# Kernel optimization log

Hardware: AMD Instinct MI355X
Metric: run time of the kernel (lower is better)

The kernel has to match this reference:

```python
import jax, jax.numpy as jnp
import numpy as np

B, T, D, H, C = 256, 512, 128, 512, 10

def setup_inputs() -> dict:
    key = jax.random.key(0)
    ks = jax.random.split(key, 16)
    def kn(k, shape):  # kaiming-normal-ish init (gain irrelevant for correctness)
        fan_in = shape[-1]
        return jax.random.normal(k, shape, dtype=jnp.float32) * (1.0 / np.sqrt(fan_in))
    return {
        "x": jax.random.randint(ks[0], (B, T), 0, 3),
        "emb": jax.random.normal(ks[1], (3, D), dtype=jnp.float32),
        "Wfx": kn(ks[2], (H, D)), "Wfh": kn(ks[3], (H, H)), "bf": jnp.zeros((H,), jnp.float32),
        "Wix": kn(ks[4], (H, D)), "Wih": kn(ks[5], (H, H)), "bi": jnp.zeros((H,), jnp.float32),
        "Wox": kn(ks[6], (H, D)), "Woh": kn(ks[7], (H, H)), "bo": jnp.zeros((H,), jnp.float32),
        "Wcx": kn(ks[8], (H, D)), "bc": jnp.zeros((H,), jnp.float32),
        "Wph": kn(ks[9], (C, H)), "bp": jnp.zeros((C,), jnp.float32),
    }

def _forward(x, emb, Wfx, Wfh, bf, Wix, Wih, bi, Wox, Woh, bo, Wcx, bc, Wph, bp):
    xe = emb[x]  # [B, T, D]
    # Precompute input-to-gate projections as one big batched matmul each.
    fx = jnp.einsum('btd,hd->bth', xe, Wfx) + bf  # [B, T, H]
    ix = jnp.einsum('btd,hd->bth', xe, Wix) + bi
    ox = jnp.einsum('btd,hd->bth', xe, Wox) + bo
    cx = jnp.einsum('btd,hd->bth', xe, Wcx) + bc
    gates = jnp.stack([fx, ix, ox, cx], axis=0).transpose(2, 1, 0, 3)  # [T, B, 4, H]

    def step(carry, g):
        c, _ = carry
        gf, gi, go, gc = g[:, 0], g[:, 1], g[:, 2], g[:, 3]  # each [B, H]
        f = jax.nn.sigmoid(gf + c @ Wfh.T)
        i = jax.nn.sigmoid(gi + c @ Wih.T)
        o = jax.nn.sigmoid(go + c @ Woh.T)
        c_new = jax.nn.sigmoid(gc) * i + c * f
        h = jnp.tanh(c_new) * o
        return (c_new, h), None

    c0 = jnp.zeros((x.shape[0], Wfh.shape[0]), jnp.float32)
    (c_fin, h_fin), _ = jax.lax.scan(step, (c0, c0), gates)
    p = h_fin @ Wph.T + bp
    return jax.nn.log_softmax(p, axis=1)

def reference(x, emb, Wfx, Wfh, bf, Wix, Wih, bi, Wox, Woh, bo, Wcx, bc, Wph, bp):
    return _forward(x, emb, Wfx, Wfh, bf, Wix, Wih, bi, Wox, Woh, bo, Wcx, bc, Wph, bp)
```

## Files before the change

kernel.cpp:

```cpp
#include <hip/hip_runtime.h>
#include <stdint.h>

#define TLEN 512
#define HDIM 512
#define DDIM 128
#define NCLS 10

typedef float f32x4 __attribute__((ext_vector_type(4)));
typedef short bf16x8 __attribute__((ext_vector_type(8)));
typedef unsigned long long u64;

__device__ __forceinline__ unsigned short f2bf(float f) {
  union { float f; unsigned u; } v; v.f = f;
  return (unsigned short)((v.u + 0x7FFFu + ((v.u >> 16) & 1u)) >> 16);
}
__device__ __forceinline__ float bf2f(unsigned short h) {
  union { unsigned u; float f; } v; v.u = ((unsigned)h) << 16; return v.f;
}
__device__ __forceinline__ float sigm(float x) {
  return __builtin_amdgcn_rcpf(1.0f + __expf(-x));
}
__device__ __forceinline__ u64 ald(const u64* p) {
  return __hip_atomic_load(p, __ATOMIC_RELAXED, __HIP_MEMORY_SCOPE_AGENT);
}
__device__ __forceinline__ void ast16(unsigned short* p, unsigned short v) {
  __hip_atomic_store(p, v, __ATOMIC_RELAXED, __HIP_MEMORY_SCOPE_AGENT);
}
__device__ __forceinline__ void astd(unsigned* p, unsigned v) {
  __hip_atomic_store(p, v, __ATOMIC_RELAXED, __HIP_MEMORY_SCOPE_AGENT);
}

__global__ void k_gates(const float* __restrict__ emb,
                        const float* __restrict__ Wfx, const float* __restrict__ bf_,
                        const float* __restrict__ Wix, const float* __restrict__ bi_,
                        const float* __restrict__ Wcx, const float* __restrict__ bc_,
                        const float* __restrict__ Wox, const float* __restrict__ bo_,
                        float* __restrict__ G) {
  int tid = blockIdx.x * 256 + threadIdx.x;
  int h = tid & (HDIM - 1);
  int v = (tid >> 9) % 3;
  int g = tid / (3 * HDIM);
  const float* W; const float* bb;
  if (g == 0)      { W = Wfx; bb = bf_; }
  else if (g == 1) { W = Wix; bb = bi_; }
  else if (g == 2) { W = Wcx; bb = bc_; }
  else             { W = Wox; bb = bo_; }
  const float* e = emb + v * DDIM;
  const float* w = W + h * DDIM;
  float s = bb[h];
  #pragma unroll 8
  for (int d = 0; d < DDIM; ++d) s += e[d] * w[d];
  if (g == 2) s = sigm(s);
  G[tid] = s;
}

__global__ void k_pack_fi(const float* __restrict__ Wfh, const float* __restrict__ Wih,
                          unsigned short* __restrict__ pk) {
  int tid = blockIdx.x * 256 + threadIdx.x;
  int l  = tid & 63;
  int kt = (tid >> 6) & 15;
  int g  = (tid >> 10) & 1;
  int nt = (tid >> 11) & 3;
  int hs = (tid >> 13) & 7;
  int n  = hs * 64 + nt * 16 + (l & 15);
  int k0 = kt * 32 + (l >> 4) * 8;
  const float* src = (g ? Wih : Wfh) + n * HDIM + k0;
  unsigned short* dst = pk + (size_t)tid * 8;
  #pragma unroll
  for (int e = 0; e < 8; ++e) dst[e] = f2bf(src[e]);
}

__global__ void k_pack_o(const float* __restrict__ Woh, unsigned short* __restrict__ pk) {
  int tid = blockIdx.x * 256 + threadIdx.x;
  int l  = tid & 63;
  int kt = (tid >> 6) & 15;
  int nt = (tid >> 10) & 3;
  int hs = (tid >> 12) & 7;
  int n  = hs * 64 + nt * 16 + (l & 15);
  int k0 = kt * 32 + (l >> 4) * 8;
  const float* src = Woh + n * HDIM + k0;
  unsigned short* dst = pk + (size_t)tid * 8;
  #pragma unroll
  for (int e = 0; e < 8; ++e) dst[e] = f2bf(src[e]);
}

__global__ __launch_bounds__(256, 1)
void k_scan(const int* __restrict__ x, const float* __restrict__ G,
            const unsigned short* __restrict__ pk2,
            const unsigned short* __restrict__ pko,
            char* __restrict__ cbuf, unsigned* __restrict__ flg,
            unsigned short* __restrict__ hfin) {
  __shared__ float gts[12][68];
  __shared__ unsigned char xv[16][516];
  __shared__ uint4 lds_a[16][64];

  const int tid  = threadIdx.x;
  const int lane = tid & 63;
  const int w    = tid >> 6;
  const int bt   = blockIdx.x & 15;
  const int hs   = blockIdx.x >> 4;

  for (int j = tid; j < 12 * 64; j += 256) {
    int gv = j >> 6, c = j & 63;
    gts[gv][c] = G[gv * HDIM + hs * 64 + c];
  }
  for (int j = tid; j < 16 * TLEN; j += 256) {
    int r = j >> 9, tt = j & (TLEN - 1);
    xv[r][tt] = (unsigned char)x[(bt * 16 + r) * TLEN + tt];
  }

  bf16x8 wf[16], wi[16];
  {
    const bf16x8* ws = (const bf16x8*)pk2 + (size_t)((hs * 4 + w) * 2) * (16 * 64) + lane;
    #pragma unroll
    for (int kt = 0; kt < 16; ++kt) { wf[kt] = ws[kt * 64]; wi[kt] = ws[(16 + kt) * 64]; }
  }

  bf16x8 afr[16];
  #pragma unroll
  for (int kt = 0; kt < 16; ++kt) afr[kt] = bf16x8{0,0,0,0,0,0,0,0};

  float cf[4] = {0.f, 0.f, 0.f, 0.f};
  const int rgrp = (lane >> 4) * 4;
  const int coll = lane & 15;
  const int col  = w * 16 + coll;
  const int colb = (hs * 64 + col) * 2;
  const int rowb = (lane & 15) * 1024 + (lane >> 4) * 16;
  const f32x4 zz = {0.f, 0.f, 0.f, 0.f};

  __syncthreads();

  for (int t = 0; t < TLEN - 1; ++t) {
    f32x4 af = zz, ai = zz;
    #pragma unroll
    for (int kt = 0; kt < 16; ++kt) {
      af = __builtin_amdgcn_mfma_f32_16x16x32_bf16(afr[kt], wf[kt], af, 0, 0, 0);
      ai = __builtin_amdgcn_mfma_f32_16x16x32_bf16(afr[kt], wi[kt], ai, 0, 0, 0);
    }
    const unsigned tg = (unsigned)(t + 1);
    const int par = (int)(tg & 1);
    char* dbase = cbuf + par * 262144 + bt * 16384;

    #pragma unroll
    for (int r = 0; r < 4; ++r) {
      int vv = xv[rgrp + r][t];
      float fg = sigm(af[r] + gts[0 + vv][col]);
      float ig = sigm(ai[r] + gts[3 + vv][col]);
      float sc = gts[6 + vv][col];
      float cn = sc * ig + cf[r] * fg;
      cf[r] = cn;
      ast16((unsigned short*)(dbase + (rgrp + r) * 1024 + colb), f2bf(cn));
    }
    __syncthreads();

    unsigned* fl = flg + (par * 16 + bt) * 16;
    if (tid == 0) astd(fl + hs, tg);

    const u64 pat2 = ((u64)tg << 32) | (u64)tg;
    const u64* fp = (const u64*)fl;
    u64 g0, g1, g2, g3;
    do {
      g0 = ald(fp + 0); g1 = ald(fp + 1); g2 = ald(fp + 2); g3 = ald(fp + 3);
    } while (((g0 ^ pat2) | (g1 ^ pat2) | (g2 ^ pat2) | (g3 ^ pat2)) != 0ULL);
    asm volatile("" ::: "memory");

    const char* rb = dbase + rowb;
    #pragma unroll
    for (int i = 0; i < 4; ++i) {
      const int kt = (w << 2) | i;
      const u64* p = (const u64*)(rb + kt * 64);
      u64 lo = ald(p + 0), hi = ald(p + 1);
      uint4 q;
      q.x = (unsigned)lo; q.y = (unsigned)(lo >> 32);
      q.z = (unsigned)hi; q.w = (unsigned)(hi >> 32);
      lds_a[kt][lane] = q;
    }
    __syncthreads();
    #pragma unroll
    for (int kt = 0; kt < 16; ++kt) {
      union { uint4 q; bf16x8 v; } u;
      u.q = lds_a[kt][lane];
      afr[kt] = u.v;
    }
  }

  {
    const int t = TLEN - 1;
    bf16x8 wo[16];
    const bf16x8* os = (const bf16x8*)pko + (size_t)(hs * 4 + w) * (16 * 64) + lane;
    #pragma unroll
    for (int kt = 0; kt < 16; ++kt) wo[kt] = os[kt * 64];
    f32x4 af = zz, ai = zz, ao = zz;
    #pragma unroll
    for (int kt = 0; kt < 16; ++kt) {
      af = __builtin_amdgcn_mfma_f32_16x16x32_bf16(afr[kt], wf[kt], af, 0, 0, 0);
      ai = __builtin_amdgcn_mfma_f32_16x16x32_bf16(afr[kt], wi[kt], ai, 0, 0, 0);
      ao = __builtin_amdgcn_mfma_f32_16x16x32_bf16(afr[kt], wo[kt], ao, 0, 0, 0);
    }
    #pragma unroll
    for (int r = 0; r < 4; ++r) {
      int vv = xv[rgrp + r][t];
      float fg = sigm(af[r] + gts[0 + vv][col]);
      float ig = sigm(ai[r] + gts[3 + vv][col]);
      float sc = gts[6 + vv][col];
      float cn = sc * ig + cf[r] * fg;
      float og = sigm(ao[r] + gts[9 + vv][col]);
      float hv = tanhf(cn) * og;
      hfin[(bt * 16 + rgrp + r) * HDIM + hs * 64 + col] = f2bf(hv);
    }
  }
}

__global__ __launch_bounds__(64)
void k_head(const unsigned short* __restrict__ hfin, const float* __restrict__ Wph,
            const float* __restrict__ bp, float* __restrict__ out) {
  const int b = blockIdx.x;
  const int lane = threadIdx.x;
  float acc[NCLS];
  #pragma unroll
  for (int c = 0; c < NCLS; ++c) acc[c] = 0.f;
  const unsigned short* hrow = hfin + (size_t)b * HDIM;
  for (int k = lane; k < HDIM; k += 64) {
    float hv = bf2f(hrow[k]);
    #pragma unroll
    for (int c = 0; c < NCLS; ++c) acc[c] += hv * Wph[c * HDIM + k];
  }
  #pragma unroll
  for (int c = 0; c < NCLS; ++c)
    #pragma unroll
    for (int off = 32; off > 0; off >>= 1)
      acc[c] += __shfl_down(acc[c], off, 64);
  if (lane == 0) {
    float p[NCLS]; float m = -1e30f;
    #pragma unroll
    for (int c = 0; c < NCLS; ++c) { p[c] = acc[c] + bp[c]; m = fmaxf(m, p[c]); }
    float s = 0.f;
    #pragma unroll
    for (int c = 0; c < NCLS; ++c) s += __expf(p[c] - m);
    const float ls = __logf(s);
    #pragma unroll
    for (int c = 0; c < NCLS; ++c) out[b * NCLS + c] = p[c] - m - ls;
  }
}

extern "C" void kernel_launch(void* const* d_in, const int* in_sizes, int n_in,
                              void* d_out, int out_size, void* d_ws, size_t ws_size,
                              hipStream_t stream) {
  const int*   x   = (const int*)d_in[0];
  const float* emb = (const float*)d_in[1];
  const float* Wfx = (const float*)d_in[2];
  const float* Wfh = (const float*)d_in[3];
  const float* bf_ = (const float*)d_in[4];
  const float* Wix = (const float*)d_in[5];
  const float* Wih = (const float*)d_in[6];
  const float* bi_ = (const float*)d_in[7];
  const float* Wox = (const float*)d_in[8];
  const float* Woh = (const float*)d_in[9];
  const float* bo_ = (const float*)d_in[10];
  const float* Wcx = (const float*)d_in[11];
  const float* bc_ = (const float*)d_in[12];
  const float* Wph = (const float*)d_in[13];
  const float* bp_ = (const float*)d_in[14];

  char* ws = (char*)d_ws;
  float*          G    = (float*)(ws);
  unsigned short* hfin = (unsigned short*)(ws + 32768);
  char*           cbuf = (char*)(ws + 524288);
  unsigned*       flg  = (unsigned*)(ws + 1048576);
  unsigned short* pk2  = (unsigned short*)(ws + 1114112);
  unsigned short* pko  = (unsigned short*)(ws + 2162688);

  hipMemsetAsync(flg, 0, 2048, stream);
  hipLaunchKernelGGL(k_gates,   dim3(24),  dim3(256), 0, stream,
                     emb, Wfx, bf_, Wix, bi_, Wcx, bc_, Wox, bo_, G);
  hipLaunchKernelGGL(k_pack_fi, dim3(256), dim3(256), 0, stream, Wfh, Wih, pk2);
  hipLaunchKernelGGL(k_pack_o,  dim3(128), dim3(256), 0, stream, Woh, pko);
  hipLaunchKernelGGL(k_scan,    dim3(128), dim3(256), 0, stream, x, G, pk2, pko, cbuf, flg, hfin);
  hipLaunchKernelGGL(k_head,    dim3(256), dim3(64),  0, stream, hfin, Wph, bp_, (float*)d_out);
}
```

Baseline: 1.469 ms.

## Replace flag barrier with step-tagged data words polled directly

Each cell-state value is now stored as a 32-bit word that holds the bf16 value with the step index in its upper half. Consumers poll the data itself with sc1 global loads until every tag matches, then pack the halves into bf16 fragments with perm. This removes the per-step __syncthreads, the flag store and the separate flag poll, cutting one round-trip of cross-block latency per timestep. The cost is twice the exchange traffic and spin-polling on the whole data tile. The final step's Woh load is also moved after the f/i MFMAs.

```diff
diff --git a/kernel.cpp b/kernel.cpp
--- a/kernel.cpp
+++ b/kernel.cpp
@@ -20,15 +20,14 @@
 __device__ __forceinline__ float sigm(float x) {
   return __builtin_amdgcn_rcpf(1.0f + __expf(-x));
 }
-__device__ __forceinline__ u64 ald(const u64* p) {
-  return __hip_atomic_load(p, __ATOMIC_RELAXED, __HIP_MEMORY_SCOPE_AGENT);
-}
-__device__ __forceinline__ void ast16(unsigned short* p, unsigned short v) {
+__device__ __forceinline__ void astw(unsigned* p, unsigned v) {
   __hip_atomic_store(p, v, __ATOMIC_RELAXED, __HIP_MEMORY_SCOPE_AGENT);
 }
-__device__ __forceinline__ void astd(unsigned* p, unsigned v) {
-  __hip_atomic_store(p, v, __ATOMIC_RELAXED, __HIP_MEMORY_SCOPE_AGENT);
-}
+
+#define GLOAD_SC1(dst, addr) \
+  asm volatile("global_load_dwordx4 %0, %1, off sc1" : "=&v"(dst) : "v"(addr))
+#define VMWAIT() do { asm volatile("s_waitcnt vmcnt(0)" ::: "memory"); \
+                      __builtin_amdgcn_sched_barrier(0); } while (0)
 
 __global__ void k_gates(const float* __restrict__ emb,
                         const float* __restrict__ Wfx, const float* __restrict__ bf_,
@@ -88,7 +87,7 @@
 void k_scan(const int* __restrict__ x, const float* __restrict__ G,
             const unsigned short* __restrict__ pk2,
             const unsigned short* __restrict__ pko,
-            char* __restrict__ cbuf, unsigned* __restrict__ flg,
+            char* __restrict__ cbuf,
             unsigned short* __restrict__ hfin) {
   __shared__ float gts[12][68];
   __shared__ unsigned char xv[16][516];
@@ -100,12 +99,12 @@
   const int bt   = blockIdx.x & 15;
   const int hs   = blockIdx.x >> 4;
 
-  for (int j = tid; j < 12 * 64; j += 256) {
-    int gv = j >> 6, c = j & 63;
+  for (int jj = tid; jj < 12 * 64; jj += 256) {
+    int gv = jj >> 6, c = jj & 63;
     gts[gv][c] = G[gv * HDIM + hs * 64 + c];
   }
-  for (int j = tid; j < 16 * TLEN; j += 256) {
-    int r = j >> 9, tt = j & (TLEN - 1);
+  for (int jj = tid; jj < 16 * TLEN; jj += 256) {
+    int r = jj >> 9, tt = jj & (TLEN - 1);
     xv[r][tt] = (unsigned char)x[(bt * 16 + r) * TLEN + tt];
   }
 
@@ -124,8 +123,10 @@
   const int rgrp = (lane >> 4) * 4;
   const int coll = lane & 15;
   const int col  = w * 16 + coll;
-  const int colb = (hs * 64 + col) * 2;
-  const int rowb = (lane & 15) * 1024 + (lane >> 4) * 16;
+  const int ktp  = 2 * hs + (col >> 5);
+  const int wrdo = col & 31;
+  const int pofs = ktp * 2048 + rgrp * 128 + wrdo * 4;
+  const int cofs = (lane & 15) * 128 + (lane >> 4) * 32;
   const f32x4 zz = {0.f, 0.f, 0.f, 0.f};
 
   __syncthreads();
@@ -137,9 +138,9 @@
       af = __builtin_amdgcn_mfma_f32_16x16x32_bf16(afr[kt], wf[kt], af, 0, 0, 0);
       ai = __builtin_amdgcn_mfma_f32_16x16x32_bf16(afr[kt], wi[kt], ai, 0, 0, 0);
     }
-    const unsigned tg = (unsigned)(t + 1);
-    const int par = (int)(tg & 1);
-    char* dbase = cbuf + par * 262144 + bt * 16384;
+    const unsigned tg  = (unsigned)(t + 1);
+    const unsigned tgh = tg << 16;
+    char* tbase = cbuf + (size_t)((tg & 1) * 16 + bt) * 32768;
 
     #pragma unroll
     for (int r = 0; r < 4; ++r) {
@@ -149,31 +150,56 @@
       float sc = gts[6 + vv][col];
       float cn = sc * ig + cf[r] * fg;
       cf[r] = cn;
-      ast16((unsigned short*)(dbase + (rgrp + r) * 1024 + colb), f2bf(cn));
-    }
-    __syncthreads();
-
-    unsigned* fl = flg + (par * 16 + bt) * 16;
-    if (tid == 0) astd(fl + hs, tg);
-
-    const u64 pat2 = ((u64)tg << 32) | (u64)tg;
-    const u64* fp = (const u64*)fl;
-    u64 g0, g1, g2, g3;
+      astw((unsigned*)(tbase + pofs + r * 128), tgh | (unsigned)f2bf(cn));
+    }
+
+    const char* qb = tbase + cofs;
+    uint4 d0, d1, d2, d3, d4, d5, d6, d7;
+    unsigned bad;
     do {
-      g0 = ald(fp + 0); g1 = ald(fp + 1); g2 = ald(fp + 2); g3 = ald(fp + 3);
-    } while (((g0 ^ pat2) | (g1 ^ pat2) | (g2 ^ pat2) | (g3 ^ pat2)) != 0ULL);
-    asm volatile("" ::: "memory");
-
-    const char* rb = dbase + rowb;
-    #pragma unroll
-    for (int i = 0; i < 4; ++i) {
-      const int kt = (w << 2) | i;
-      const u64* p = (const u64*)(rb + kt * 64);
-      u64 lo = ald(p + 0), hi = ald(p + 1);
+      GLOAD_SC1(d0, qb + ((w << 2) | 0) * 2048);
+      GLOAD_SC1(d1, qb + ((w << 2) | 0) * 2048 + 16);
+      GLOAD_SC1(d2, qb + ((w << 2) | 1) * 2048);
+      GLOAD_SC1(d3, qb + ((w << 2) | 1) * 2048 + 16);
+      GLOAD_SC1(d4, qb + ((w << 2) | 2) * 2048);
+      GLOAD_SC1(d5, qb + ((w << 2) | 2) * 2048 + 16);
+      GLOAD_SC1(d6, qb + ((w << 2) | 3) * 2048);
+      GLOAD_SC1(d7, qb + ((w << 2) | 3) * 2048 + 16);
+      VMWAIT();
+      unsigned m = 0;
+      m |= (d0.x ^ tgh) | (d0.y ^ tgh) | (d0.z ^ tgh) | (d0.w ^ tgh);
+      m |= (d1.x ^ tgh) | (d1.y ^ tgh) | (d1.z ^ tgh) | (d1.w ^ tgh);
+      m |= (d2.x ^ tgh) | (d2.y ^ tgh) | (d2.z ^ tgh) | (d2.w ^ tgh);
+      m |= (d3.x ^ tgh) | (d3.y ^ tgh) | (d3.z ^ tgh) | (d3.w ^ tgh);
+      m |= (d4.x ^ tgh) | (d4.y ^ tgh) | (d4.z ^ tgh) | (d4.w ^ tgh);
+      m |= (d5.x ^ tgh) | (d5.y ^ tgh) | (d5.z ^ tgh) | (d5.w ^ tgh);
+      m |= (d6.x ^ tgh) | (d6.y ^ tgh) | (d6.z ^ tgh) | (d6.w ^ tgh);
+      m |= (d7.x ^ tgh) | (d7.y ^ tgh) | (d7.z ^ tgh) | (d7.w ^ tgh);
+      bad = m & 0xFFFF0000u;
+    } while (__any(bad != 0));
+
+    {
       uint4 q;
-      q.x = (unsigned)lo; q.y = (unsigned)(lo >> 32);
-      q.z = (unsigned)hi; q.w = (unsigned)(hi >> 32);
-      lds_a[kt][lane] = q;
+      q.x = __builtin_amdgcn_perm(d0.y, d0.x, 0x05040100);
+      q.y = __builtin_amdgcn_perm(d0.w, d0.z, 0x05040100);
+      q.z = __builtin_amdgcn_perm(d1.y, d1.x, 0x05040100);
+      q.w = __builtin_amdgcn_perm(d1.w, d1.z, 0x05040100);
+      lds_a[(w << 2) | 0][lane] = q;
+      q.x = __builtin_amdgcn_perm(d2.y, d2.x, 0x05040100);
+      q.y = __builtin_amdgcn_perm(d2.w, d2.z, 0x05040100);
+      q.z = __builtin_amdgcn_perm(d3.y, d3.x, 0x05040100);
+      q.w = __builtin_amdgcn_perm(d3.w, d3.z, 0x05040100);
+      lds_a[(w << 2) | 1][lane] = q;
+      q.x = __builtin_amdgcn_perm(d4.y, d4.x, 0x05040100);
+      q.y = __builtin_amdgcn_perm(d4.w, d4.z, 0x05040100);
+      q.z = __builtin_amdgcn_perm(d5.y, d5.x, 0x05040100);
+      q.w = __builtin_amdgcn_perm(d5.w, d5.z, 0x05040100);
+      lds_a[(w << 2) | 2][lane] = q;
+      q.x = __builtin_amdgcn_perm(d6.y, d6.x, 0x05040100);
+      q.y = __builtin_amdgcn_perm(d6.w, d6.z, 0x05040100);
+      q.z = __builtin_amdgcn_perm(d7.y, d7.x, 0x05040100);
+      q.w = __builtin_amdgcn_perm(d7.w, d7.z, 0x05040100);
+      lds_a[(w << 2) | 3][lane] = q;
     }
     __syncthreads();
     #pragma unroll
@@ -186,17 +212,19 @@
 
   {
     const int t = TLEN - 1;
-    bf16x8 wo[16];
-    const bf16x8* os = (const bf16x8*)pko + (size_t)(hs * 4 + w) * (16 * 64) + lane;
-    #pragma unroll
-    for (int kt = 0; kt < 16; ++kt) wo[kt] = os[kt * 64];
     f32x4 af = zz, ai = zz, ao = zz;
     #pragma unroll
     for (int kt = 0; kt < 16; ++kt) {
       af = __builtin_amdgcn_mfma_f32_16x16x32_bf16(afr[kt], wf[kt], af, 0, 0, 0);
       ai = __builtin_amdgcn_mfma_f32_16x16x32_bf16(afr[kt], wi[kt], ai, 0, 0, 0);
+    }
+    bf16x8 wo[16];
+    const bf16x8* os = (const bf16x8*)pko + (size_t)(hs * 4 + w) * (16 * 64) + lane;
+    #pragma unroll
+    for (int kt = 0; kt < 16; ++kt) wo[kt] = os[kt * 64];
+    #pragma unroll
+    for (int kt = 0; kt < 16; ++kt)
       ao = __builtin_amdgcn_mfma_f32_16x16x32_bf16(afr[kt], wo[kt], ao, 0, 0, 0);
-    }
     #pragma unroll
     for (int r = 0; r < 4; ++r) {
       int vv = xv[rgrp + r][t];
@@ -266,15 +294,14 @@
   float*          G    = (float*)(ws);
   unsigned short* hfin = (unsigned short*)(ws + 32768);
   char*           cbuf = (char*)(ws + 524288);
-  unsigned*       flg  = (unsigned*)(ws + 1048576);
-  unsigned short* pk2  = (unsigned short*)(ws + 1114112);
-  unsigned short* pko  = (unsigned short*)(ws + 2162688);
-
-  hipMemsetAsync(flg, 0, 2048, stream);
+  unsigned short* pk2  = (unsigned short*)(ws + 1572864);
+  unsigned short* pko  = (unsigned short*)(ws + 2621440);
+
   hipLaunchKernelGGL(k_gates,   dim3(24),  dim3(256), 0, stream,
                      emb, Wfx, bf_, Wix, bi_, Wcx, bc_, Wox, bo_, G);
   hipLaunchKernelGGL(k_pack_fi, dim3(256), dim3(256), 0, stream, Wfh, Wih, pk2);
   hipLaunchKernelGGL(k_pack_o,  dim3(128), dim3(256), 0, stream, Woh, pko);
-  hipLaunchKernelGGL(k_scan,    dim3(128), dim3(256), 0, stream, x, G, pk2, pko, cbuf, flg, hfin);
+  hipLaunchKernelGGL(k_scan,    dim3(128), dim3(256), 0, stream,
+                     x, G, pk2, pko, cbuf, hfin);
   hipLaunchKernelGGL(k_head,    dim3(256), dim3(64),  0, stream, hfin, Wph, bp_, (float*)d_out);
 }
```

Result: slower. 2.012 ms (+37.0%).

## Add XCD-local fast path for inter-block step synchronization and state exchange

Applied to the files above, without the earlier changes.

At startup each block records its XCC_ID and checks whether all 8 blocks sharing a batch tile run on the same XCD. If they do, the cell state and step flags are also written and polled with sc0 (L2-coherent, XCD-local) loads and stores. This is meant to avoid the higher-latency device-scope path on every one of the 511 timesteps. A bounded spin falls back to a mirrored sc1/agent-scope buffer, which adds an extra store per element and relies on hardware-specific cache-scope semantics. The Woh load is also moved after the f/i MFMAs in the final step.

```diff
diff --git a/kernel.cpp b/kernel.cpp
--- a/kernel.cpp
+++ b/kernel.cpp
@@ -20,15 +20,26 @@
 __device__ __forceinline__ float sigm(float x) {
   return __builtin_amdgcn_rcpf(1.0f + __expf(-x));
 }
-__device__ __forceinline__ u64 ald(const u64* p) {
-  return __hip_atomic_load(p, __ATOMIC_RELAXED, __HIP_MEMORY_SCOPE_AGENT);
-}
 __device__ __forceinline__ void ast16(unsigned short* p, unsigned short v) {
   __hip_atomic_store(p, v, __ATOMIC_RELAXED, __HIP_MEMORY_SCOPE_AGENT);
 }
 __device__ __forceinline__ void astd(unsigned* p, unsigned v) {
   __hip_atomic_store(p, v, __ATOMIC_RELAXED, __HIP_MEMORY_SCOPE_AGENT);
 }
+__device__ __forceinline__ unsigned aldd(const unsigned* p) {
+  return __hip_atomic_load(p, __ATOMIC_RELAXED, __HIP_MEMORY_SCOPE_AGENT);
+}
+
+#define GLOAD_SC1(dst, addr) \
+  asm volatile("global_load_dwordx4 %0, %1, off sc1" : "=&v"(dst) : "v"(addr))
+#define GLOAD_SC0(dst, addr) \
+  asm volatile("global_load_dwordx4 %0, %1, off sc0" : "=&v"(dst) : "v"(addr))
+#define GSTORE16_SC0(addr, val) \
+  asm volatile("global_store_short %0, %1, off sc0" :: "v"(addr), "v"(val) : "memory")
+#define GSTORED_SC0(addr, val) \
+  asm volatile("global_store_dword %0, %1, off sc0" :: "v"(addr), "v"(val) : "memory")
+#define VMWAIT() do { asm volatile("s_waitcnt vmcnt(0)" ::: "memory"); \
+                      __builtin_amdgcn_sched_barrier(0); } while (0)
 
 __global__ void k_gates(const float* __restrict__ emb,
                         const float* __restrict__ Wfx, const float* __restrict__ bf_,
@@ -88,11 +99,14 @@
 void k_scan(const int* __restrict__ x, const float* __restrict__ G,
             const unsigned short* __restrict__ pk2,
             const unsigned short* __restrict__ pko,
-            char* __restrict__ cbuf, unsigned* __restrict__ flg,
+            char* __restrict__ bufB, unsigned* __restrict__ flgB,
+            char* __restrict__ bufA, unsigned* __restrict__ flgA,
+            unsigned* __restrict__ xcdtab,
             unsigned short* __restrict__ hfin) {
   __shared__ float gts[12][68];
   __shared__ unsigned char xv[16][516];
   __shared__ uint4 lds_a[16][64];
+  __shared__ int fastsh, fastok;
 
   const int tid  = threadIdx.x;
   const int lane = tid & 63;
@@ -100,12 +114,25 @@
   const int bt   = blockIdx.x & 15;
   const int hs   = blockIdx.x >> 4;
 
-  for (int j = tid; j < 12 * 64; j += 256) {
-    int gv = j >> 6, c = j & 63;
+  if (tid == 0) {
+    unsigned myx;
+    asm volatile("s_getreg_b32 %0, hwreg(HW_REG_XCC_ID)" : "=s"(myx));
+    astd(xcdtab + (hs * 16 + bt), (myx & 0xFFu) | 0x100u);
+    unsigned id0 = 0; int f = 1;
+    for (int k = 0; k < 8; ++k) {
+      unsigned v;
+      do { v = aldd(xcdtab + (k * 16 + bt)); } while (!(v & 0x100u));
+      if (k == 0) id0 = v; else f &= (v == id0);
+    }
+    fastsh = f; fastok = f;
+  }
+
+  for (int jj = tid; jj < 12 * 64; jj += 256) {
+    int gv = jj >> 6, c = jj & 63;
     gts[gv][c] = G[gv * HDIM + hs * 64 + c];
   }
-  for (int j = tid; j < 16 * TLEN; j += 256) {
-    int r = j >> 9, tt = j & (TLEN - 1);
+  for (int jj = tid; jj < 16 * TLEN; jj += 256) {
+    int r = jj >> 9, tt = jj & (TLEN - 1);
     xv[r][tt] = (unsigned char)x[(bt * 16 + r) * TLEN + tt];
   }
 
@@ -139,7 +166,9 @@
     }
     const unsigned tg = (unsigned)(t + 1);
     const int par = (int)(tg & 1);
-    char* dbase = cbuf + par * 262144 + bt * 16384;
+    char* dbB = bufB + par * 262144 + bt * 16384;
+    char* dbA = bufA + par * 262144 + bt * 16384;
+    const bool tryfast = (fastok != 0);
 
     #pragma unroll
     for (int r = 0; r < 4; ++r) {
@@ -149,32 +178,52 @@
       float sc = gts[6 + vv][col];
       float cn = sc * ig + cf[r] * fg;
       cf[r] = cn;
-      ast16((unsigned short*)(dbase + (rgrp + r) * 1024 + colb), f2bf(cn));
+      unsigned short hv = f2bf(cn);
+      ast16((unsigned short*)(dbB + (rgrp + r) * 1024 + colb), hv);
+      GSTORE16_SC0(dbA + (rgrp + r) * 1024 + colb, (unsigned)hv);
     }
     __syncthreads();
 
-    unsigned* fl = flg + (par * 16 + bt) * 16;
-    if (tid == 0) astd(fl + hs, tg);
-
-    const u64 pat2 = ((u64)tg << 32) | (u64)tg;
-    const u64* fp = (const u64*)fl;
-    u64 g0, g1, g2, g3;
-    do {
-      g0 = ald(fp + 0); g1 = ald(fp + 1); g2 = ald(fp + 2); g3 = ald(fp + 3);
-    } while (((g0 ^ pat2) | (g1 ^ pat2) | (g2 ^ pat2) | (g3 ^ pat2)) != 0ULL);
-    asm volatile("" ::: "memory");
-
-    const char* rb = dbase + rowb;
-    #pragma unroll
-    for (int i = 0; i < 4; ++i) {
-      const int kt = (w << 2) | i;
-      const u64* p = (const u64*)(rb + kt * 64);
-      u64 lo = ald(p + 0), hi = ald(p + 1);
-      uint4 q;
-      q.x = (unsigned)lo; q.y = (unsigned)(lo >> 32);
-      q.z = (unsigned)hi; q.w = (unsigned)(hi >> 32);
-      lds_a[kt][lane] = q;
-    }
+    unsigned* flB = flgB + (par * 16 + bt) * 16;
+    unsigned* flA = flgA + (par * 16 + bt) * 16;
+    if (tid == 0) {
+      GSTORED_SC0(flA + hs, tg);
+      astd(flB + hs, tg);
+    }
+
+    uint4 f0, f1;
+    bool ok = false;
+    if (tryfast) {
+      for (int it = 0; it < 24; ++it) {
+        GLOAD_SC0(f0, (const char*)flA); GLOAD_SC0(f1, (const char*)flA + 16); VMWAIT();
+        if (((f0.x ^ tg) | (f0.y ^ tg) | (f0.z ^ tg) | (f0.w ^ tg) |
+             (f1.x ^ tg) | (f1.y ^ tg) | (f1.z ^ tg) | (f1.w ^ tg)) == 0u) {
+          ok = true; break;
+        }
+      }
+      if (!ok && lane == 0) fastok = 0;
+    }
+    if (!ok) {
+      do { GLOAD_SC1(f0, (const char*)flB); GLOAD_SC1(f1, (const char*)flB + 16); VMWAIT(); }
+      while (((f0.x ^ tg) | (f0.y ^ tg) | (f0.z ^ tg) | (f0.w ^ tg) |
+              (f1.x ^ tg) | (f1.y ^ tg) | (f1.z ^ tg) | (f1.w ^ tg)) != 0u);
+    }
+
+    uint4 q0, q1, q2, q3;
+    if (ok) {
+      const char* rb = dbA + rowb + (w << 8);
+      GLOAD_SC0(q0, rb);       GLOAD_SC0(q1, rb + 64);
+      GLOAD_SC0(q2, rb + 128); GLOAD_SC0(q3, rb + 192);
+    } else {
+      const char* rb = dbB + rowb + (w << 8);
+      GLOAD_SC1(q0, rb);       GLOAD_SC1(q1, rb + 64);
+      GLOAD_SC1(q2, rb + 128); GLOAD_SC1(q3, rb + 192);
+    }
+    VMWAIT();
+    lds_a[(w << 2) | 0][lane] = q0;
+    lds_a[(w << 2) | 1][lane] = q1;
+    lds_a[(w << 2) | 2][lane] = q2;
+    lds_a[(w << 2) | 3][lane] = q3;
     __syncthreads();
     #pragma unroll
     for (int kt = 0; kt < 16; ++kt) {
@@ -186,17 +235,19 @@
 
   {
     const int t = TLEN - 1;
-    bf16x8 wo[16];
-    const bf16x8* os = (const bf16x8*)pko + (size_t)(hs * 4 + w) * (16 * 64) + lane;
-    #pragma unroll
-    for (int kt = 0; kt < 16; ++kt) wo[kt] = os[kt * 64];
     f32x4 af = zz, ai = zz, ao = zz;
     #pragma unroll
     for (int kt = 0; kt < 16; ++kt) {
       af = __builtin_amdgcn_mfma_f32_16x16x32_bf16(afr[kt], wf[kt], af, 0, 0, 0);
       ai = __builtin_amdgcn_mfma_f32_16x16x32_bf16(afr[kt], wi[kt], ai, 0, 0, 0);
+    }
+    bf16x8 wo[16];
+    const bf16x8* os = (const bf16x8*)pko + (size_t)(hs * 4 + w) * (16 * 64) + lane;
+    #pragma unroll
+    for (int kt = 0; kt < 16; ++kt) wo[kt] = os[kt * 64];
+    #pragma unroll
+    for (int kt = 0; kt < 16; ++kt)
       ao = __builtin_amdgcn_mfma_f32_16x16x32_bf16(afr[kt], wo[kt], ao, 0, 0, 0);
-    }
     #pragma unroll
     for (int r = 0; r < 4; ++r) {
       int vv = xv[rgrp + r][t];
@@ -263,18 +314,22 @@
   const float* bp_ = (const float*)d_in[14];
 
   char* ws = (char*)d_ws;
-  float*          G    = (float*)(ws);
-  unsigned short* hfin = (unsigned short*)(ws + 32768);
-  char*           cbuf = (char*)(ws + 524288);
-  unsigned*       flg  = (unsigned*)(ws + 1048576);
-  unsigned short* pk2  = (unsigned short*)(ws + 1114112);
-  unsigned short* pko  = (unsigned short*)(ws + 2162688);
-
-  hipMemsetAsync(flg, 0, 2048, stream);
+  float*          G      = (float*)(ws);
+  unsigned*       flgB   = (unsigned*)(ws + 24576);
+  unsigned*       flgA   = (unsigned*)(ws + 26624);
+  unsigned*       xcdtab = (unsigned*)(ws + 28672);
+  unsigned short* hfin   = (unsigned short*)(ws + 32768);
+  char*           bufA   = (char*)(ws + 327680);
+  char*           bufB   = (char*)(ws + 1048576);
+  unsigned short* pk2    = (unsigned short*)(ws + 1572864);
+  unsigned short* pko    = (unsigned short*)(ws + 2621440);
+
+  hipMemsetAsync(flgB, 0, 8192, stream);
   hipLaunchKernelGGL(k_gates,   dim3(24),  dim3(256), 0, stream,
                      emb, Wfx, bf_, Wix, bi_, Wcx, bc_, Wox, bo_, G);
   hipLaunchKernelGGL(k_pack_fi, dim3(256), dim3(256), 0, stream, Wfh, Wih, pk2);
   hipLaunchKernelGGL(k_pack_o,  dim3(128), dim3(256), 0, stream, Woh, pko);
-  hipLaunchKernelGGL(k_scan,    dim3(128), dim3(256), 0, stream, x, G, pk2, pko, cbuf, flg, hfin);
+  hipLaunchKernelGGL(k_scan,    dim3(128), dim3(256), 0, stream,
+                     x, G, pk2, pko, bufB, flgB, bufA, flgA, xcdtab, hfin);
   hipLaunchKernelGGL(k_head,    dim3(256), dim3(64),  0, stream, hfin, Wph, bp_, (float*)d_out);
 }
```

Result: faster. 1.234 ms (-16.0%).

## Split scan across 256 blocks with 8-row batch groups and sc1 polling

Applied to the files above, without the earlier changes.

Doubles the scan grid to 256 blocks, so each block handles 8 batch rows instead of 16. The MFMA tiles still cover 16 rows, so half the lanes are masked off and the upper rows are zero-padded in LDS. The cell-state exchange buffer moves to a new layout, and flag polling switches from atomic 64-bit loads to pipelined inline-asm dwordx4 loads with sc1 and double-buffered outstanding requests. This aims to spread the serial recurrence over more CUs and cut the per-step latency of flag and state exchange. The cost is wasted MFMA work, and correctness now depends on the sc1 cache semantics.

```diff
diff --git a/kernel.cpp b/kernel.cpp
--- a/kernel.cpp
+++ b/kernel.cpp
@@ -8,7 +8,6 @@
 
 typedef float f32x4 __attribute__((ext_vector_type(4)));
 typedef short bf16x8 __attribute__((ext_vector_type(8)));
-typedef unsigned long long u64;
 
 __device__ __forceinline__ unsigned short f2bf(float f) {
   union { float f; unsigned u; } v; v.f = f;
@@ -20,15 +19,21 @@
 __device__ __forceinline__ float sigm(float x) {
   return __builtin_amdgcn_rcpf(1.0f + __expf(-x));
 }
-__device__ __forceinline__ u64 ald(const u64* p) {
-  return __hip_atomic_load(p, __ATOMIC_RELAXED, __HIP_MEMORY_SCOPE_AGENT);
-}
 __device__ __forceinline__ void ast16(unsigned short* p, unsigned short v) {
   __hip_atomic_store(p, v, __ATOMIC_RELAXED, __HIP_MEMORY_SCOPE_AGENT);
 }
 __device__ __forceinline__ void astd(unsigned* p, unsigned v) {
   __hip_atomic_store(p, v, __ATOMIC_RELAXED, __HIP_MEMORY_SCOPE_AGENT);
 }
+
+#define GLOAD_SC1(dst, addr) \
+  asm volatile("global_load_dwordx4 %0, %1, off sc1" : "=&v"(dst) : "v"(addr))
+#define VMWAIT() do { asm volatile("s_waitcnt vmcnt(0)" ::: "memory"); \
+                      __builtin_amdgcn_sched_barrier(0); } while (0)
+#define VMWAIT2() do { asm volatile("s_waitcnt vmcnt(2)" ::: "memory"); \
+                       __builtin_amdgcn_sched_barrier(0); } while (0)
+#define CHK(a, b) ((((a).x ^ tg) | ((a).y ^ tg) | ((a).z ^ tg) | ((a).w ^ tg) | \
+                    ((b).x ^ tg) | ((b).y ^ tg) | ((b).z ^ tg) | ((b).w ^ tg)) == 0u)
 
 __global__ void k_gates(const float* __restrict__ emb,
                         const float* __restrict__ Wfx, const float* __restrict__ bf_,
@@ -91,23 +96,25 @@
             char* __restrict__ cbuf, unsigned* __restrict__ flg,
             unsigned short* __restrict__ hfin) {
   __shared__ float gts[12][68];
-  __shared__ unsigned char xv[16][516];
+  __shared__ unsigned char xv[8][512];
   __shared__ uint4 lds_a[16][64];
 
   const int tid  = threadIdx.x;
   const int lane = tid & 63;
   const int w    = tid >> 6;
-  const int bt   = blockIdx.x & 15;
-  const int hs   = blockIdx.x >> 4;
-
-  for (int j = tid; j < 12 * 64; j += 256) {
-    int gv = j >> 6, c = j & 63;
+  const int hs   = blockIdx.x & 7;
+  const int btg  = blockIdx.x >> 3;
+
+  for (int jj = tid; jj < 12 * 64; jj += 256) {
+    int gv = jj >> 6, c = jj & 63;
     gts[gv][c] = G[gv * HDIM + hs * 64 + c];
   }
-  for (int j = tid; j < 16 * TLEN; j += 256) {
-    int r = j >> 9, tt = j & (TLEN - 1);
-    xv[r][tt] = (unsigned char)x[(bt * 16 + r) * TLEN + tt];
-  }
+  for (int jj = tid; jj < 8 * 512; jj += 256) {
+    int r = jj >> 9, tt = jj & 511;
+    xv[r][tt] = (unsigned char)x[(btg * 8 + r) * TLEN + tt];
+  }
+  for (int jj = tid; jj < 16 * 64; jj += 256)
+    ((uint4*)lds_a)[jj] = uint4{0, 0, 0, 0};
 
   bf16x8 wf[16], wi[16];
   {
@@ -124,8 +131,10 @@
   const int rgrp = (lane >> 4) * 4;
   const int coll = lane & 15;
   const int col  = w * 16 + coll;
-  const int colb = (hs * 64 + col) * 2;
-  const int rowb = (lane & 15) * 1024 + (lane >> 4) * 16;
+  const int gcol = hs * 64 + col;
+  const int soff = (gcol >> 5) * 512 + (gcol & 31) * 2;
+  const int aoff = (lane & 7) * 64 + (lane >> 4) * 16;
+  const bool act = (lane < 32);
   const f32x4 zz = {0.f, 0.f, 0.f, 0.f};
 
   __syncthreads();
@@ -139,42 +148,56 @@
     }
     const unsigned tg = (unsigned)(t + 1);
     const int par = (int)(tg & 1);
-    char* dbase = cbuf + par * 262144 + bt * 16384;
-
-    #pragma unroll
-    for (int r = 0; r < 4; ++r) {
-      int vv = xv[rgrp + r][t];
-      float fg = sigm(af[r] + gts[0 + vv][col]);
-      float ig = sigm(ai[r] + gts[3 + vv][col]);
-      float sc = gts[6 + vv][col];
-      float cn = sc * ig + cf[r] * fg;
-      cf[r] = cn;
-      ast16((unsigned short*)(dbase + (rgrp + r) * 1024 + colb), f2bf(cn));
+    char* dbase = cbuf + (size_t)(par * 32 + btg) * 8192;
+
+    if (act) {
+      #pragma unroll
+      for (int r = 0; r < 4; ++r) {
+        const int rr = rgrp + r;
+        int vv = xv[rr][t];
+        float fg = sigm(af[r] + gts[0 + vv][col]);
+        float ig = sigm(ai[r] + gts[3 + vv][col]);
+        float sc = gts[6 + vv][col];
+        float cn = sc * ig + cf[r] * fg;
+        cf[r] = cn;
+        ast16((unsigned short*)(dbase + soff + rr * 64), f2bf(cn));
+      }
     }
     __syncthreads();
 
-    unsigned* fl = flg + (par * 16 + bt) * 16;
+    unsigned* fl = flg + (par * 32 + btg) * 16;
     if (tid == 0) astd(fl + hs, tg);
 
-    const u64 pat2 = ((u64)tg << 32) | (u64)tg;
-    const u64* fp = (const u64*)fl;
-    u64 g0, g1, g2, g3;
-    do {
-      g0 = ald(fp + 0); g1 = ald(fp + 1); g2 = ald(fp + 2); g3 = ald(fp + 3);
-    } while (((g0 ^ pat2) | (g1 ^ pat2) | (g2 ^ pat2) | (g3 ^ pat2)) != 0ULL);
-    asm volatile("" ::: "memory");
-
-    const char* rb = dbase + rowb;
-    #pragma unroll
-    for (int i = 0; i < 4; ++i) {
-      const int kt = (w << 2) | i;
-      const u64* p = (const u64*)(rb + kt * 64);
-      u64 lo = ald(p + 0), hi = ald(p + 1);
-      uint4 q;
-      q.x = (unsigned)lo; q.y = (unsigned)(lo >> 32);
-      q.z = (unsigned)hi; q.w = (unsigned)(hi >> 32);
-      lds_a[kt][lane] = q;
-    }
+    const char* fb = (const char*)fl;
+    uint4 fa0, fa1, fb0, fb1;
+    bool got = false;
+    GLOAD_SC1(fa0, fb); GLOAD_SC1(fa1, fb + 16);
+    GLOAD_SC1(fb0, fb); GLOAD_SC1(fb1, fb + 16);
+    for (int it = 0; it < 64; ++it) {
+      VMWAIT2();
+      if (CHK(fa0, fa1)) { got = true; break; }
+      GLOAD_SC1(fa0, fb); GLOAD_SC1(fa1, fb + 16);
+      VMWAIT2();
+      if (CHK(fb0, fb1)) { got = true; break; }
+      GLOAD_SC1(fb0, fb); GLOAD_SC1(fb1, fb + 16);
+    }
+    VMWAIT();
+    if (!got) {
+      do { GLOAD_SC1(fa0, fb); GLOAD_SC1(fa1, fb + 16); VMWAIT(); }
+      while (!CHK(fa0, fa1));
+    }
+
+    const char* rb = dbase + aoff;
+    uint4 q0, q1, q2, q3;
+    GLOAD_SC1(q0, rb + (4 * w + 0) * 512);
+    GLOAD_SC1(q1, rb + (4 * w + 1) * 512);
+    GLOAD_SC1(q2, rb + (4 * w + 2) * 512);
+    GLOAD_SC1(q3, rb + (4 * w + 3) * 512);
+    VMWAIT();
+    lds_a[(w << 2) | 0][lane] = q0;
+    lds_a[(w << 2) | 1][lane] = q1;
+    lds_a[(w << 2) | 2][lane] = q2;
+    lds_a[(w << 2) | 3][lane] = q3;
     __syncthreads();
     #pragma unroll
     for (int kt = 0; kt < 16; ++kt) {
@@ -186,27 +209,32 @@
 
   {
     const int t = TLEN - 1;
-    bf16x8 wo[16];
-    const bf16x8* os = (const bf16x8*)pko + (size_t)(hs * 4 + w) * (16 * 64) + lane;
-    #pragma unroll
-    for (int kt = 0; kt < 16; ++kt) wo[kt] = os[kt * 64];
     f32x4 af = zz, ai = zz, ao = zz;
     #pragma unroll
     for (int kt = 0; kt < 16; ++kt) {
       af = __builtin_amdgcn_mfma_f32_16x16x32_bf16(afr[kt], wf[kt], af, 0, 0, 0);
       ai = __builtin_amdgcn_mfma_f32_16x16x32_bf16(afr[kt], wi[kt], ai, 0, 0, 0);
+    }
+    bf16x8 wo[16];
+    const bf16x8* os = (const bf16x8*)pko + (size_t)(hs * 4 + w) * (16 * 64) + lane;
+    #pragma unroll
+    for (int kt = 0; kt < 16; ++kt) wo[kt] = os[kt * 64];
+    #pragma unroll
+    for (int kt = 0; kt < 16; ++kt)
       ao = __builtin_amdgcn_mfma_f32_16x16x32_bf16(afr[kt], wo[kt], ao, 0, 0, 0);
-    }
-    #pragma unroll
-    for (int r = 0; r < 4; ++r) {
-      int vv = xv[rgrp + r][t];
-      float fg = sigm(af[r] + gts[0 + vv][col]);
-      float ig = sigm(ai[r] + gts[3 + vv][col]);
-      float sc = gts[6 + vv][col];
-      float cn = sc * ig + cf[r] * fg;
-      float og = sigm(ao[r] + gts[9 + vv][col]);
-      float hv = tanhf(cn) * og;
-      hfin[(bt * 16 + rgrp + r) * HDIM + hs * 64 + col] = f2bf(hv);
+    if (act) {
+      #pragma unroll
+      for (int r = 0; r < 4; ++r) {
+        const int rr = rgrp + r;
+        int vv = xv[rr][t];
+        float fg = sigm(af[r] + gts[0 + vv][col]);
+        float ig = sigm(ai[r] + gts[3 + vv][col]);
+        float sc = gts[6 + vv][col];
+        float cn = sc * ig + cf[r] * fg;
+        float og = sigm(ao[r] + gts[9 + vv][col]);
+        float hv = tanhf(cn) * og;
+        hfin[(btg * 8 + rr) * HDIM + gcol] = f2bf(hv);
+      }
     }
   }
 }
@@ -264,17 +292,18 @@
 
   char* ws = (char*)d_ws;
   float*          G    = (float*)(ws);
+  unsigned*       flg  = (unsigned*)(ws + 24576);
   unsigned short* hfin = (unsigned short*)(ws + 32768);
   char*           cbuf = (char*)(ws + 524288);
-  unsigned*       flg  = (unsigned*)(ws + 1048576);
-  unsigned short* pk2  = (unsigned short*)(ws + 1114112);
-  unsigned short* pko  = (unsigned short*)(ws + 2162688);
-
-  hipMemsetAsync(flg, 0, 2048, stream);
+  unsigned short* pk2  = (unsigned short*)(ws + 1572864);
+  unsigned short* pko  = (unsigned short*)(ws + 2621440);
+
+  hipMemsetAsync(flg, 0, 4096, stream);
   hipLaunchKernelGGL(k_gates,   dim3(24),  dim3(256), 0, stream,
                      emb, Wfx, bf_, Wix, bi_, Wcx, bc_, Wox, bo_, G);
   hipLaunchKernelGGL(k_pack_fi, dim3(256), dim3(256), 0, stream, Wfh, Wih, pk2);
   hipLaunchKernelGGL(k_pack_o,  dim3(128), dim3(256), 0, stream, Woh, pko);
-  hipLaunchKernelGGL(k_scan,    dim3(128), dim3(256), 0, stream, x, G, pk2, pko, cbuf, flg, hfin);
+  hipLaunchKernelGGL(k_scan,    dim3(256), dim3(256), 0, stream,
+                     x, G, pk2, pko, cbuf, flg, hfin);
   hipLaunchKernelGGL(k_head,    dim3(256), dim3(64),  0, stream, hfin, Wph, bp_, (float*)d_out);
 }
```

After: 1.461 ms. No clear change (-0.5%).
